# Kernel tuning notes

Measured on AMD Instinct MI355X. Metric: run time of the kernel, lower is better.

## Reference

```python
import jax, jax.numpy as jnp
import numpy as np

N = 8192      # nodes
DIN = 128     # in_channels
DH = 64       # hidden_channels (dim_out, num_heads=1)
DOUT = 32     # out_channels
RATIO = 0.5
K_KEEP = int(np.ceil(RATIO * N))  # SAGPooling keep count (single graph)
LN_EPS = 1e-5


def _linear_params(k, fan_in, fan_out):
    kw, kb = jax.random.split(k)
    W = jax.random.normal(kw, (fan_in, fan_out), dtype=jnp.float32) / jnp.sqrt(jnp.float32(fan_in))
    b = jax.random.normal(kb, (fan_out,), dtype=jnp.float32) * 0.01
    return W, b


def setup_inputs() -> dict:
    key = jax.random.key(0)
    ks = jax.random.split(key, 8)
    x = jax.random.normal(ks[0], (N, DIN), dtype=jnp.float32)
    batch = jnp.zeros((N,), dtype=jnp.int64)  # single graph
    Wq, bq = _linear_params(ks[1], DIN, DH)
    Wk, bk = _linear_params(ks[2], DIN, DH)
    Wv, bv = _linear_params(ks[3], DIN, DH)
    gcn_W, gcn_b = _linear_params(ks[4], DH, DH)       # GCNConv weight/bias
    score_W, score_b = _linear_params(ks[5], DH, 1)    # SAGPooling score GCNConv
    ln_g = jnp.ones((DH,), dtype=jnp.float32)
    ln_b = jnp.zeros((DH,), dtype=jnp.float32)
    head_W, head_b = _linear_params(ks[6], DH, DOUT)
    return dict(x=x, batch=batch, Wq=Wq, bq=bq, Wk=Wk, bk=bk, Wv=Wv, bv=bv,
                gcn_W=gcn_W, gcn_b=gcn_b, score_W=score_W, score_b=score_b,
                ln_g=ln_g, ln_b=ln_b, head_W=head_W, head_b=head_b)


def _forward(x, Wq, bq, Wk, bk, Wv, bv, gcn_W, gcn_b, score_W, score_b,
             ln_g, ln_b, head_W, head_b):
    # --- self-attention over all nodes (num_heads = 1) ---
    Q = x @ Wq + bq                                        # [N, DH]
    K = x @ Wk + bk
    V = x @ Wv + bv
    attn = jax.nn.softmax(Q @ K.T / jnp.sqrt(jnp.float32(DH)), axis=-1)  # [N, N]
    h = attn @ V                                           # [N, DH]

    # --- edge construction: threshold attention, ensure self-loops ---
    # (attn > 0.5).nonzero() -> edge set; empty -> self-loop fallback; then
    # add_self_loops. Dense equivalent: A = max(mask, I).
    eye = jnp.eye(N, dtype=x.dtype)
    A = jnp.maximum((attn > 0.5).astype(x.dtype), eye)     # [N, N], diag = 1

    # symmetric GCN normalization  D^{-1/2} A D^{-1/2}
    dinv = jax.lax.rsqrt(A.sum(axis=1))                    # [N]
    An = dinv[:, None] * A * dinv[None, :]                 # [N, N]

    # --- GCNConv layer ---
    g = An @ (h @ gcn_W) + gcn_b                           # [N, DH]

    # --- SAGPooling: GCNConv scorer -> tanh -> global top-k (single graph) ---
    score = jnp.tanh((An @ (g @ score_W) + score_b).squeeze(-1))  # [N]
    top_scores, perm = jax.lax.top_k(score, K_KEEP)        # sorted desc, like PyG topk
    xp = g[perm] * top_scores[:, None]                     # [K, DH], multiplier = 1

    # --- LayerNorm + ReLU (dropout is identity in eval) ---
    mu = xp.mean(axis=-1, keepdims=True)
    var = xp.var(axis=-1, keepdims=True)
    xp = (xp - mu) * jax.lax.rsqrt(var + LN_EPS) * ln_g + ln_b
    xp = jax.nn.relu(xp)

    # --- prediction head ---
    return xp @ head_W + head_b                            # [K, DOUT]


def reference(x, batch, Wq, bq, Wk, bk, Wv, bv, gcn_W, gcn_b,
              score_W, score_b, ln_g, ln_b, head_W, head_b):
    del batch  # single graph; grouping has no effect on the math
    return _forward(x, Wq, bq, Wk, bk, Wv, bv, gcn_W, gcn_b,
                    score_W, score_b, ln_g, ln_b, head_W, head_b)
```

## Files before the change

### kernel.cpp

```cpp
#include <hip/hip_runtime.h>
#include <hip/hip_bf16.h>
#include <cstdio>

typedef __hip_bfloat16 bf16;
typedef __attribute__((ext_vector_type(8))) short v8s;
typedef __attribute__((ext_vector_type(4))) short v4s;
typedef __attribute__((ext_vector_type(4))) float v4f;
typedef __attribute__((ext_vector_type(4))) double v4d;

#define MFMA16(a, b, c) __builtin_amdgcn_mfma_f32_16x16x32_bf16((a), (b), (c), 0, 0, 0)

#define NN 8192
#define DIN 128
#define DH 64
#define DOUT 32
#define KKEEP 4096
#define SPLITS 8
#define SPATT 8

__device__ __forceinline__ float bf2f(bf16 v) { return __bfloat162float(v); }
__device__ __forceinline__ short f2bfs(float f) {
  __hip_bfloat16 h = __float2bfloat16(f);
  return *reinterpret_cast<short*>(&h);
}
__device__ __forceinline__ bf16 f2bf(float v) { return __float2bfloat16(v); }

__device__ __forceinline__ double exp_d(double s) {
  const double L2E    = 1.4426950408889634074;
  const double LN2_HI = 6.93147180369123816490e-01;
  const double LN2_LO = 1.90821492927058770002e-10;
  double t  = s * L2E;
  double kf = rint(t);
  double r  = fma(-kf, LN2_HI, s);
  r = fma(-kf, LN2_LO, r);
  double p = 1.0 / 362880.0;
  p = fma(p, r, 1.0 / 40320.0);
  p = fma(p, r, 1.0 / 5040.0);
  p = fma(p, r, 1.0 / 720.0);
  p = fma(p, r, 1.0 / 120.0);
  p = fma(p, r, 1.0 / 24.0);
  p = fma(p, r, 1.0 / 6.0);
  p = fma(p, r, 0.5);
  p = fma(p, r, 1.0);
  p = fma(p, r, 1.0);
  int k = (int)kf;
  long long bits = ((long long)(1023 + k)) << 52;
  double sc = __longlong_as_double(bits);
  return p * sc;
}

__global__ void k0_ucb(const float* __restrict__ gW, const float* __restrict__ sW,
                       const float* __restrict__ gb, double* __restrict__ u) {
  int c = threadIdx.x;
  double acc = 0.0, accb = 0.0;
  for (int d = 0; d < DH; ++d) {
    double swd = (double)sW[d];
    acc  = fma((double)gW[c * DH + d], swd, acc);
    accb = fma((double)gb[d], swd, accb);
  }
  u[c] = acc;
  if (c == 0) u[64] = accb;
}

__global__ __launch_bounds__(256) void k1_prep(
    const float* __restrict__ x, const float* __restrict__ Wq, const float* __restrict__ bq,
    const float* __restrict__ Wk, const float* __restrict__ bk, const float* __restrict__ Wv,
    const float* __restrict__ bv, const double* __restrict__ u,
    double* __restrict__ Qd, double* __restrict__ Kd, double* __restrict__ w,
    bf16* __restrict__ Qb, bf16* __restrict__ Kb, bf16* __restrict__ Vt) {
  __shared__ double xs[16][DIN];
  int t = threadIdx.x;
  int nb = blockIdx.x * 16;
  for (int idx = t; idx < 16 * DIN; idx += 256)
    xs[idx >> 7][idx & 127] = (double)x[(size_t)nb * DIN + idx];
  __syncthreads();
  int d = t & 63;
  int sub = t >> 6;
  double bqd = (double)bq[d];
  double bkd = (double)bk[d];
  double bvd = (double)bv[d];
  double ud = u[d];
  for (int pass = 0; pass < 4; ++pass) {
    int n = pass * 4 + sub;
    double aq = bqd, ak = bkd, av = bvd;
#pragma unroll 8
    for (int c = 0; c < DIN; ++c) {
      double xv = xs[n][c];
      aq = fma(xv, (double)Wq[c * DH + d], aq);
      ak = fma(xv, (double)Wk[c * DH + d], ak);
      av = fma(xv, (double)Wv[c * DH + d], av);
    }
    aq *= 0.125;
    int node = nb + n;
    Qd[(size_t)node * DH + d] = aq;
    Kd[(size_t)node * DH + d] = ak;
    Qb[(size_t)node * DH + d] = f2bf((float)aq);
    Kb[(size_t)node * DH + d] = f2bf((float)ak);
    Vt[(size_t)d * NN + node] = f2bf((float)av);
    double pw = av * ud;
#pragma unroll
    for (int off = 32; off; off >>= 1) pw += __shfl_xor(pw, off);
    if (d == 0) w[node] = pw;
  }
}

__global__ __launch_bounds__(256) void k2_scores(
    const double* __restrict__ Qd, const double* __restrict__ Kd, const double* __restrict__ w,
    double* __restrict__ Zp, double* __restrict__ Wp, double* __restrict__ Ep, int* __restrict__ Jp) {
  __shared__ __align__(16) double Kbuf[2][32][66];
  const int t = threadIdx.x;
  const int wv = t >> 6;
  const int l = t & 63;
  const int li = l & 15, lg = l >> 4;
  const int rb = (blockIdx.x & 127) * 64;
  const int sp = blockIdx.x >> 7;
  const int cbeg = sp * (NN / SPLITS);

  double qreg[16];
  const double* qrow = Qd + (size_t)(rb + 16 * wv + li) * DH + lg;
#pragma unroll
  for (int tt = 0; tt < 16; ++tt) qreg[tt] = qrow[4 * tt];

  {
    const double* src = Kd + (size_t)cbeg * DH;
#pragma unroll
    for (int k = 0; k < 4; ++k) {
      int g = t + 256 * k;
      int r = g >> 5, c2 = g & 31;
      *(double2*)&Kbuf[0][r][c2 * 2] = *(const double2*)&src[r * DH + c2 * 2];
    }
  }
  __syncthreads();

  double Zt[4] = {0, 0, 0, 0}, Wt[4] = {0, 0, 0, 0}, Et[4] = {-1, -1, -1, -1};
  int Jt[4] = {0, 0, 0, 0};

  const int NT = (NN / SPLITS) / 32;
  for (int kt = 0; kt < NT; ++kt) {
    const int buf = kt & 1;
    if (kt + 1 < NT) {
      const double* src = Kd + (size_t)(cbeg + (kt + 1) * 32) * DH;
#pragma unroll
      for (int k = 0; k < 4; ++k) {
        int g = t + 256 * k;
        int r = g >> 5, c2 = g & 31;
        *(double2*)&Kbuf[buf ^ 1][r][c2 * 2] = *(const double2*)&src[r * DH + c2 * 2];
      }
    }
#pragma unroll
    for (int hf = 0; hf < 2; ++hf) {
      v4d acc = (v4d){0.0, 0.0, 0.0, 0.0};
#pragma unroll
      for (int tt = 0; tt < 16; ++tt) {
        double bfrag = Kbuf[buf][li + 16 * hf][4 * tt + lg];
        acc = __builtin_amdgcn_mfma_f64_16x16x4f64(qreg[tt], bfrag, acc, 0, 0, 0);
      }
      const int col = cbeg + kt * 32 + 16 * hf + li;
      const double wj = w[col];
#pragma unroll
      for (int v = 0; v < 4; ++v) {
        double e = exp_d(acc[v]);
        Zt[v] += e;
        Wt[v] = fma(e, wj, Wt[v]);
        if (e > Et[v]) { Et[v] = e; Jt[v] = col; }
      }
    }
    __syncthreads();
  }

#pragma unroll
  for (int v = 0; v < 4; ++v) {
#pragma unroll
    for (int m = 1; m < 16; m <<= 1) {
      Zt[v] += __shfl_xor(Zt[v], m);
      Wt[v] += __shfl_xor(Wt[v], m);
      double e2 = __shfl_xor(Et[v], m);
      int j2 = __shfl_xor(Jt[v], m);
      if (e2 > Et[v] || (e2 == Et[v] && j2 < Jt[v])) { Et[v] = e2; Jt[v] = j2; }
    }
  }
  if (li == 0) {
#pragma unroll
    for (int v = 0; v < 4; ++v) {
      int row = rb + 16 * wv + lg + 4 * v;
      Zp[sp * NN + row] = Zt[v];
      Wp[sp * NN + row] = Wt[v];
      Ep[sp * NN + row] = Et[v];
      Jp[sp * NN + row] = Jt[v];
    }
  }
}

__global__ void k3_combine(const double* __restrict__ Zp, const double* __restrict__ Wp,
                           const double* __restrict__ Ep, const int* __restrict__ Jp,
                           double* __restrict__ tau, int* __restrict__ extra, int* __restrict__ jmA) {
  int i = blockIdx.x * 256 + threadIdx.x;
  double Z = 0, W = 0, E = -1;
  int J = 0;
  for (int sp = 0; sp < SPLITS; ++sp) {
    Z += Zp[sp * NN + i];
    W += Wp[sp * NN + i];
    double e = Ep[sp * NN + i];
    if (e > E || (e == E && Jp[sp * NN + i] < J)) { E = e; J = Jp[sp * NN + i]; }
  }
  tau[i] = W / Z;
  extra[i] = (E > 0.5 * Z) && (J != i);
  jmA[i] = J & (NN - 1);
}

__global__ __launch_bounds__(256) void k4_mfma(const bf16* __restrict__ Qb, const bf16* __restrict__ Kb,
                                               const bf16* __restrict__ Vt,
                                               float* __restrict__ hp, float* __restrict__ zp) {
  __shared__ __align__(16) short P[4][16 * 40];
  const int t = threadIdx.x;
  const int wv = t >> 6;
  const int l = t & 63, g = l >> 4, li = l & 15;
  const int qb = (blockIdx.x & 127) * 64 + wv * 16;
  const int sp = blockIdx.x >> 7;
  short* Pw = &P[wv][0];
  const v8s q0 = *(const v8s*)(Qb + (size_t)(qb + li) * DH + g * 8);
  const v8s q1 = *(const v8s*)(Qb + (size_t)(qb + li) * DH + 32 + g * 8);
  v4f hacc[4];
#pragma unroll
  for (int db = 0; db < 4; ++db) hacc[db] = (v4f){0.f, 0.f, 0.f, 0.f};
  float zl = 0.f;
  const int kbeg = sp * (NN / SPATT);
  for (int jb = kbeg; jb < kbeg + NN / SPATT; jb += 32) {
    const bf16* kp = Kb + (size_t)(jb + li) * DH + g * 8;
    v8s ka0 = *(const v8s*)(kp);
    v8s ka1 = *(const v8s*)(kp + 32);
    v8s kb0 = *(const v8s*)(kp + 16 * DH);
    v8s kb1 = *(const v8s*)(kp + 16 * DH + 32);
    v4f c0 = (v4f){0.f, 0.f, 0.f, 0.f}, c1 = (v4f){0.f, 0.f, 0.f, 0.f};
    c0 = MFMA16(ka0, q0, c0);
    c0 = MFMA16(ka1, q1, c0);
    c1 = MFMA16(kb0, q0, c1);
    c1 = MFMA16(kb1, q1, c1);
    v4s p0, p1;
#pragma unroll
    for (int r = 0; r < 4; ++r) {
      short b0 = f2bfs(__expf(c0[r]));
      short b1 = f2bfs(__expf(c1[r]));
      p0[r] = b0;
      p1[r] = b1;
      zl += bf2f(*reinterpret_cast<bf16*>(&b0));
      zl += bf2f(*reinterpret_cast<bf16*>(&b1));
    }
    *(v4s*)&Pw[li * 40 + g * 4] = p0;
    *(v4s*)&Pw[li * 40 + 16 + g * 4] = p1;
    __syncthreads();
    v8s pf = *(const v8s*)&Pw[li * 40 + g * 8];
#pragma unroll
    for (int db = 0; db < 4; ++db) {
      const v8s vb = *(const v8s*)(Vt + (size_t)(db * 16 + li) * NN + jb + g * 8);
      hacc[db] = MFMA16(pf, vb, hacc[db]);
    }
    __syncthreads();
  }
  zl += __shfl_xor(zl, 16);
  zl += __shfl_xor(zl, 32);
  if (g == 0) zp[sp * NN + qb + li] = zl;
#pragma unroll
  for (int r = 0; r < 4; ++r) {
    int row = qb + g * 4 + r;
#pragma unroll
    for (int db = 0; db < 4; ++db)
      hp[((size_t)sp * NN + row) * DH + db * 16 + li] = hacc[db][r];
  }
}

__global__ __launch_bounds__(256) void k9_hM(const float* __restrict__ hp, const float* __restrict__ zp,
                                             const float* __restrict__ gW, float* __restrict__ M) {
  __shared__ float xs[4][DH];
  int t = threadIdx.x;
  int sub = t >> 6, d = t & 63;
  int n = blockIdx.x * 4 + sub;
  float Z = 0.f, H = 0.f;
#pragma unroll
  for (int sp = 0; sp < SPATT; ++sp) {
    Z += zp[sp * NN + n];
    H += hp[((size_t)sp * NN + n) * DH + d];
  }
  xs[sub][d] = H / Z;
  __syncthreads();
  float acc = 0.f;
#pragma unroll 8
  for (int c = 0; c < DH; ++c) acc = fmaf(xs[sub][c], gW[c * DH + d], acc);
  M[(size_t)n * DH + d] = acc;
}

__global__ void k5_t(const double* __restrict__ tau, const int* __restrict__ extra,
                     const int* __restrict__ jmA, const double* __restrict__ u, double* __restrict__ tarr) {
  int i = blockIdx.x * 256 + threadIdx.x;
  int ex = extra[i];
  double di = ex ? 0.70710678118654752440 : 1.0;
  double acc = di * tau[i];
  if (ex) {
    int j = jmA[i] & (NN - 1);
    double dj = extra[j] ? 0.70710678118654752440 : 1.0;
    acc = fma(dj, tau[j], acc);
  }
  tarr[i] = fma(di, acc, u[64]);
}

__global__ void k6_pre(const double* __restrict__ tarr, const int* __restrict__ extra,
                       const int* __restrict__ jmA, const float* __restrict__ score_b,
                       double* __restrict__ pre, float* __restrict__ sc32, int* __restrict__ cnt) {
  int i = blockIdx.x * 256 + threadIdx.x;
  int ex = extra[i];
  double di = ex ? 0.70710678118654752440 : 1.0;
  double acc = di * tarr[i];
  if (ex) {
    int j = jmA[i] & (NN - 1);
    double dj = extra[j] ? 0.70710678118654752440 : 1.0;
    acc = fma(dj, tarr[j], acc);
  }
  double p = fma(di, acc, (double)score_b[0]);
  pre[i] = p;
  sc32[i] = (float)tanh(p);
  cnt[i] = 0;
}

__global__ void k7_rank(const double* __restrict__ pre, int* __restrict__ cnt) {
  int i = (blockIdx.x & 31) * 256 + threadIdx.x;
  int j0 = (blockIdx.x >> 5) * 512;
  double si = pre[i];
  int c = 0;
#pragma unroll 4
  for (int j = j0; j < j0 + 512; j += 2) {
    double2 pj = *(const double2*)(pre + j);
    c += (pj.x > si || (pj.x == si && j < i));
    c += (pj.y > si || (pj.y == si && (j + 1) < i));
  }
  atomicAdd(&cnt[i], c);
}

__global__ void k8_sel(const int* __restrict__ cnt, int* __restrict__ sel) {
  int i = blockIdx.x * 256 + threadIdx.x;
  unsigned r = (unsigned)cnt[i];
  if (r < KKEEP) sel[r] = i;
}

__global__ __launch_bounds__(256) void k11_head(const float* __restrict__ M, const int* __restrict__ extra,
                                                const int* __restrict__ jmA, const float* __restrict__ gb,
                                                const float* __restrict__ sc32, const int* __restrict__ sel,
                                                const float* __restrict__ lg, const float* __restrict__ lb,
                                                const float* __restrict__ hW, const float* __restrict__ hb,
                                                float* __restrict__ out) {
  __shared__ float xs[4][DH];
  int t = threadIdx.x;
  int wv = t >> 6, d = t & 63;
  int p = blockIdx.x * 4 + wv;
  int i = sel[p] & (NN - 1);
  int ex = extra[i];
  float di = ex ? 0.70710678f : 1.0f;
  float acc0 = di * M[(size_t)i * DH + d];
  if (ex) {
    int j = jmA[i] & (NN - 1);
    acc0 = fmaf(extra[j] ? 0.70710678f : 1.0f, M[(size_t)j * DH + d], acc0);
  }
  float gval = fmaf(di, acc0, gb[d]);
  float v = gval * sc32[i];
  float s1 = v;
#pragma unroll
  for (int off = 32; off; off >>= 1) s1 += __shfl_xor(s1, off);
  float mu = s1 * (1.0f / 64.0f);
  float dv = v - mu;
  float s2 = dv * dv;
#pragma unroll
  for (int off = 32; off; off >>= 1) s2 += __shfl_xor(s2, off);
  float var = s2 * (1.0f / 64.0f);
  float xn = dv * rsqrtf(var + 1e-5f) * lg[d] + lb[d];
  xs[wv][d] = fmaxf(xn, 0.0f);
  __syncthreads();
  if (t < 128) {
    int r = t >> 5, o = t & 31;
    float acc = hb[o];
#pragma unroll 8
    for (int c = 0; c < DH; ++c) acc = fmaf(xs[r][c], hW[c * DOUT + o], acc);
    out[(size_t)(blockIdx.x * 4 + r) * DOUT + o] = acc;
  }
}

#define MB 1048576ull
constexpr size_t OFF_QD   = 0 * MB;
constexpr size_t OFF_KD   = 4 * MB;
constexpr size_t OFF_M    = 16 * MB;
constexpr size_t OFF_ZP   = 20 * MB;
constexpr size_t OFF_WP   = 21 * MB;
constexpr size_t OFF_EP   = 22 * MB;
constexpr size_t OFF_JP   = 23 * MB;
constexpr size_t OFF_W    = 24 * MB;
constexpr size_t OFF_U    = 25 * MB;
constexpr size_t OFF_TAU  = 26 * MB;
constexpr size_t OFF_EX   = 27 * MB;
constexpr size_t OFF_JM   = 28 * MB;
constexpr size_t OFF_T    = 29 * MB;
constexpr size_t OFF_PRE  = 30 * MB;
constexpr size_t OFF_SC   = 31 * MB;
constexpr size_t OFF_CNT  = 32 * MB;
constexpr size_t OFF_SEL  = 33 * MB;
constexpr size_t OFF_HP   = 34 * MB;
constexpr size_t OFF_ZATT = 50 * MB;
constexpr size_t OFF_QB   = 51 * MB;
constexpr size_t OFF_KB   = 52 * MB;
constexpr size_t OFF_VT   = 53 * MB;
constexpr size_t WS_NEEDED = 54 * MB;

extern "C" void kernel_launch(void* const* d_in, const int* in_sizes, int n_in,
                              void* d_out, int out_size, void* d_ws, size_t ws_size,
                              hipStream_t stream) {
  if (n_in < 16 || ws_size < WS_NEEDED || out_size != KKEEP * DOUT) {
    fprintf(stderr, "[sag] GUARD ws=%zu need=%zu n_in=%d out=%d\n", ws_size, WS_NEEDED, n_in, out_size);
    return;
  }
  const float* x   = (const float*)d_in[0];
  const float* Wq  = (const float*)d_in[2];
  const float* bq  = (const float*)d_in[3];
  const float* Wk  = (const float*)d_in[4];
  const float* bk  = (const float*)d_in[5];
  const float* Wv  = (const float*)d_in[6];
  const float* bv  = (const float*)d_in[7];
  const float* gW  = (const float*)d_in[8];
  const float* gb  = (const float*)d_in[9];
  const float* sW  = (const float*)d_in[10];
  const float* sb  = (const float*)d_in[11];
  const float* lg  = (const float*)d_in[12];
  const float* lb  = (const float*)d_in[13];
  const float* hW  = (const float*)d_in[14];
  const float* hb  = (const float*)d_in[15];
  float* out = (float*)d_out;

  char* ws = (char*)d_ws;
  double* Qd  = (double*)(ws + OFF_QD);
  double* Kd  = (double*)(ws + OFF_KD);
  bf16*   Qb  = (bf16*)(ws + OFF_QB);
  bf16*   Kb  = (bf16*)(ws + OFF_KB);
  bf16*   Vt  = (bf16*)(ws + OFF_VT);
  float*  M   = (float*)(ws + OFF_M);
  double* Zp  = (double*)(ws + OFF_ZP);
  double* Wp  = (double*)(ws + OFF_WP);
  double* Ep  = (double*)(ws + OFF_EP);
  int*    Jp  = (int*)(ws + OFF_JP);
  double* w   = (double*)(ws + OFF_W);
  double* u   = (double*)(ws + OFF_U);
  double* tau = (double*)(ws + OFF_TAU);
  int*    ex  = (int*)(ws + OFF_EX);
  int*    jm  = (int*)(ws + OFF_JM);
  double* tarr= (double*)(ws + OFF_T);
  double* pre = (double*)(ws + OFF_PRE);
  float*  sc32= (float*)(ws + OFF_SC);
  int*    cnt = (int*)(ws + OFF_CNT);
  int*    sel = (int*)(ws + OFF_SEL);
  float*  hp  = (float*)(ws + OFF_HP);
  float*  zatt= (float*)(ws + OFF_ZATT);

  hipLaunchKernelGGL(k0_ucb, dim3(1), dim3(64), 0, stream, gW, sW, gb, u);
  hipLaunchKernelGGL(k1_prep, dim3(512), dim3(256), 0, stream, x, Wq, bq, Wk, bk, Wv, bv, u,
                     Qd, Kd, w, Qb, Kb, Vt);
  hipLaunchKernelGGL(k2_scores, dim3(128 * SPLITS), dim3(256), 0, stream, Qd, Kd, w, Zp, Wp, Ep, Jp);
  hipLaunchKernelGGL(k3_combine, dim3(32), dim3(256), 0, stream, Zp, Wp, Ep, Jp, tau, ex, jm);
  hipLaunchKernelGGL(k4_mfma, dim3(128 * SPATT), dim3(256), 0, stream, Qb, Kb, Vt, hp, zatt);
  hipLaunchKernelGGL(k9_hM, dim3(2048), dim3(256), 0, stream, hp, zatt, gW, M);
  hipLaunchKernelGGL(k5_t, dim3(32), dim3(256), 0, stream, tau, ex, jm, u, tarr);
  hipLaunchKernelGGL(k6_pre, dim3(32), dim3(256), 0, stream, tarr, ex, jm, sb, pre, sc32, cnt);
  hipLaunchKernelGGL(k7_rank, dim3(512), dim3(256), 0, stream, pre, cnt);
  hipLaunchKernelGGL(k8_sel, dim3(32), dim3(256), 0, stream, cnt, sel);
  hipLaunchKernelGGL(k11_head, dim3(1024), dim3(256), 0, stream, M, ex, jm, gb, sc32, sel,
                     lg, lb, hW, hb, out);
}
```

Before: 407.5 us.

## Fuse fp64 score and bf16 attention kernels into one interleaved launch

Merges the fp64 MFMA score kernel and the bf16 attention-times-V kernel into one launch. Even blocks run the score work and odd blocks run the attention work, so the fp64-heavy and bf16-heavy blocks can share CUs at the same time. The fp64 path's K tile is halved from 32 to 16 rows so shared memory fits the common buffer, which doubles its loop trips and barriers. Occupancy may drop because register pressure is now the maximum of both paths.

After: 487.0 us. 1.19x slower.

```diff
diff --git a/kernel.cpp b/kernel.cpp
--- a/kernel.cpp
+++ b/kernel.cpp
@@ -104,58 +104,56 @@
   }
 }
 
-__global__ __launch_bounds__(256) void k2_scores(
+__global__ __launch_bounds__(256) void k24_fused(
     const double* __restrict__ Qd, const double* __restrict__ Kd, const double* __restrict__ w,
-    double* __restrict__ Zp, double* __restrict__ Wp, double* __restrict__ Ep, int* __restrict__ Jp) {
-  __shared__ __align__(16) double Kbuf[2][32][66];
+    double* __restrict__ Zp, double* __restrict__ Wp, double* __restrict__ Ep, int* __restrict__ Jp,
+    const bf16* __restrict__ Qb, const bf16* __restrict__ Kb, const bf16* __restrict__ Vt,
+    float* __restrict__ hp, float* __restrict__ zp) {
+  __shared__ __align__(16) char smem[16896];
   const int t = threadIdx.x;
   const int wv = t >> 6;
   const int l = t & 63;
-  const int li = l & 15, lg = l >> 4;
-  const int rb = (blockIdx.x & 127) * 64;
-  const int sp = blockIdx.x >> 7;
-  const int cbeg = sp * (NN / SPLITS);
-
-  double qreg[16];
-  const double* qrow = Qd + (size_t)(rb + 16 * wv + li) * DH + lg;
-#pragma unroll
-  for (int tt = 0; tt < 16; ++tt) qreg[tt] = qrow[4 * tt];
-
-  {
-    const double* src = Kd + (size_t)cbeg * DH;
-#pragma unroll
-    for (int k = 0; k < 4; ++k) {
-      int g = t + 256 * k;
-      int r = g >> 5, c2 = g & 31;
-      *(double2*)&Kbuf[0][r][c2 * 2] = *(const double2*)&src[r * DH + c2 * 2];
-    }
-  }
-  __syncthreads();
-
-  double Zt[4] = {0, 0, 0, 0}, Wt[4] = {0, 0, 0, 0}, Et[4] = {-1, -1, -1, -1};
-  int Jt[4] = {0, 0, 0, 0};
-
-  const int NT = (NN / SPLITS) / 32;
-  for (int kt = 0; kt < NT; ++kt) {
-    const int buf = kt & 1;
-    if (kt + 1 < NT) {
-      const double* src = Kd + (size_t)(cbeg + (kt + 1) * 32) * DH;
-#pragma unroll
-      for (int k = 0; k < 4; ++k) {
-        int g = t + 256 * k;
-        int r = g >> 5, c2 = g & 31;
-        *(double2*)&Kbuf[buf ^ 1][r][c2 * 2] = *(const double2*)&src[r * DH + c2 * 2];
-      }
-    }
-#pragma unroll
-    for (int hf = 0; hf < 2; ++hf) {
+  const int sub = blockIdx.x >> 1;
+
+  if ((blockIdx.x & 1) == 0) {
+    double (*Kbuf)[16][66] = (double (*)[16][66])smem;
+    const int li = l & 15, lg = l >> 4;
+    const int rb = (sub & 127) * 64;
+    const int sp = sub >> 7;
+    const int cbeg = sp * (NN / SPLITS);
+
+    double qreg[16];
+    const double* qrow = Qd + (size_t)(rb + 16 * wv + li) * DH + lg;
+#pragma unroll
+    for (int tt = 0; tt < 16; ++tt) qreg[tt] = qrow[4 * tt];
+
+    {
+      const double* src = Kd + (size_t)cbeg * DH;
+      int r = t >> 4, c = (t & 15) * 4;
+      *(double2*)&Kbuf[0][r][c]     = *(const double2*)&src[r * DH + c];
+      *(double2*)&Kbuf[0][r][c + 2] = *(const double2*)&src[r * DH + c + 2];
+    }
+    __syncthreads();
+
+    double Zt[4] = {0, 0, 0, 0}, Wt[4] = {0, 0, 0, 0}, Et[4] = {-1, -1, -1, -1};
+    int Jt[4] = {0, 0, 0, 0};
+
+    const int NT = (NN / SPLITS) / 16;
+    for (int kt = 0; kt < NT; ++kt) {
+      const int buf = kt & 1;
+      if (kt + 1 < NT) {
+        const double* src = Kd + (size_t)(cbeg + (kt + 1) * 16) * DH;
+        int r = t >> 4, c = (t & 15) * 4;
+        *(double2*)&Kbuf[buf ^ 1][r][c]     = *(const double2*)&src[r * DH + c];
+        *(double2*)&Kbuf[buf ^ 1][r][c + 2] = *(const double2*)&src[r * DH + c + 2];
+      }
       v4d acc = (v4d){0.0, 0.0, 0.0, 0.0};
 #pragma unroll
       for (int tt = 0; tt < 16; ++tt) {
-        double bfrag = Kbuf[buf][li + 16 * hf][4 * tt + lg];
+        double bfrag = Kbuf[buf][li][4 * tt + lg];
         acc = __builtin_amdgcn_mfma_f64_16x16x4f64(qreg[tt], bfrag, acc, 0, 0, 0);
       }
-      const int col = cbeg + kt * 32 + 16 * hf + li;
+      const int col = cbeg + kt * 16 + li;
       const double wj = w[col];
 #pragma unroll
       for (int v = 0; v < 4; ++v) {
@@ -164,29 +162,84 @@
         Wt[v] = fma(e, wj, Wt[v]);
         if (e > Et[v]) { Et[v] = e; Jt[v] = col; }
       }
-    }
-    __syncthreads();
-  }
-
-#pragma unroll
-  for (int v = 0; v < 4; ++v) {
-#pragma unroll
-    for (int m = 1; m < 16; m <<= 1) {
-      Zt[v] += __shfl_xor(Zt[v], m);
-      Wt[v] += __shfl_xor(Wt[v], m);
-      double e2 = __shfl_xor(Et[v], m);
-      int j2 = __shfl_xor(Jt[v], m);
-      if (e2 > Et[v] || (e2 == Et[v] && j2 < Jt[v])) { Et[v] = e2; Jt[v] = j2; }
-    }
-  }
-  if (li == 0) {
+      __syncthreads();
+    }
+
 #pragma unroll
     for (int v = 0; v < 4; ++v) {
-      int row = rb + 16 * wv + lg + 4 * v;
-      Zp[sp * NN + row] = Zt[v];
-      Wp[sp * NN + row] = Wt[v];
-      Ep[sp * NN + row] = Et[v];
-      Jp[sp * NN + row] = Jt[v];
+#pragma unroll
+      for (int m = 1; m < 16; m <<= 1) {
+        Zt[v] += __shfl_xor(Zt[v], m);
+        Wt[v] += __shfl_xor(Wt[v], m);
+        double e2 = __shfl_xor(Et[v], m);
+        int j2 = __shfl_xor(Jt[v], m);
+        if (e2 > Et[v] || (e2 == Et[v] && j2 < Jt[v])) { Et[v] = e2; Jt[v] = j2; }
+      }
+    }
+    if (li == 0) {
+#pragma unroll
+      for (int v = 0; v < 4; ++v) {
+        int row = rb + 16 * wv + lg + 4 * v;
+        Zp[sp * NN + row] = Zt[v];
+        Wp[sp * NN + row] = Wt[v];
+        Ep[sp * NN + row] = Et[v];
+        Jp[sp * NN + row] = Jt[v];
+      }
+    }
+  } else {
+    short (*P)[16 * 40] = (short (*)[16 * 40])smem;
+    const int g = l >> 4, li = l & 15;
+    const int qb = (sub & 127) * 64 + wv * 16;
+    const int sp = sub >> 7;
+    short* Pw = &P[wv][0];
+    const v8s q0 = *(const v8s*)(Qb + (size_t)(qb + li) * DH + g * 8);
+    const v8s q1 = *(const v8s*)(Qb + (size_t)(qb + li) * DH + 32 + g * 8);
+    v4f hacc[4];
+#pragma unroll
+    for (int db = 0; db < 4; ++db) hacc[db] = (v4f){0.f, 0.f, 0.f, 0.f};
+    float zl = 0.f;
+    const int kbeg = sp * (NN / SPATT);
+    for (int jb = kbeg; jb < kbeg + NN / SPATT; jb += 32) {
+      const bf16* kp = Kb + (size_t)(jb + li) * DH + g * 8;
+      v8s ka0 = *(const v8s*)(kp);
+      v8s ka1 = *(const v8s*)(kp + 32);
+      v8s kb0 = *(const v8s*)(kp + 16 * DH);
+      v8s kb1 = *(const v8s*)(kp + 16 * DH + 32);
+      v4f c0 = (v4f){0.f, 0.f, 0.f, 0.f}, c1 = (v4f){0.f, 0.f, 0.f, 0.f};
+      c0 = MFMA16(ka0, q0, c0);
+      c0 = MFMA16(ka1, q1, c0);
+      c1 = MFMA16(kb0, q0, c1);
+      c1 = MFMA16(kb1, q1, c1);
+      v4s p0, p1;
+#pragma unroll
+      for (int r = 0; r < 4; ++r) {
+        short b0 = f2bfs(__expf(c0[r]));
+        short b1 = f2bfs(__expf(c1[r]));
+        p0[r] = b0;
+        p1[r] = b1;
+        zl += bf2f(*reinterpret_cast<bf16*>(&b0));
+        zl += bf2f(*reinterpret_cast<bf16*>(&b1));
+      }
+      *(v4s*)&Pw[li * 40 + g * 4] = p0;
+      *(v4s*)&Pw[li * 40 + 16 + g * 4] = p1;
+      __syncthreads();
+      v8s pf = *(const v8s*)&Pw[li * 40 + g * 8];
+#pragma unroll
+      for (int db = 0; db < 4; ++db) {
+        const v8s vb = *(const v8s*)(Vt + (size_t)(db * 16 + li) * NN + jb + g * 8);
+        hacc[db] = MFMA16(pf, vb, hacc[db]);
+      }
+      __syncthreads();
+    }
+    zl += __shfl_xor(zl, 16);
+    zl += __shfl_xor(zl, 32);
+    if (g == 0) zp[sp * NN + qb + li] = zl;
+#pragma unroll
+    for (int r = 0; r < 4; ++r) {
+      int row = qb + g * 4 + r;
+#pragma unroll
+      for (int db = 0; db < 4; ++db)
+        hp[((size_t)sp * NN + row) * DH + db * 16 + li] = hacc[db][r];
     }
   }
 }
@@ -206,67 +259,6 @@
   tau[i] = W / Z;
   extra[i] = (E > 0.5 * Z) && (J != i);
   jmA[i] = J & (NN - 1);
-}
-
-__global__ __launch_bounds__(256) void k4_mfma(const bf16* __restrict__ Qb, const bf16* __restrict__ Kb,
-                                               const bf16* __restrict__ Vt,
-                                               float* __restrict__ hp, float* __restrict__ zp) {
-  __shared__ __align__(16) short P[4][16 * 40];
-  const int t = threadIdx.x;
-  const int wv = t >> 6;
-  const int l = t & 63, g = l >> 4, li = l & 15;
-  const int qb = (blockIdx.x & 127) * 64 + wv * 16;
-  const int sp = blockIdx.x >> 7;
-  short* Pw = &P[wv][0];
-  const v8s q0 = *(const v8s*)(Qb + (size_t)(qb + li) * DH + g * 8);
-  const v8s q1 = *(const v8s*)(Qb + (size_t)(qb + li) * DH + 32 + g * 8);
-  v4f hacc[4];
-#pragma unroll
-  for (int db = 0; db < 4; ++db) hacc[db] = (v4f){0.f, 0.f, 0.f, 0.f};
-  float zl = 0.f;
-  const int kbeg = sp * (NN / SPATT);
-  for (int jb = kbeg; jb < kbeg + NN / SPATT; jb += 32) {
-    const bf16* kp = Kb + (size_t)(jb + li) * DH + g * 8;
-    v8s ka0 = *(const v8s*)(kp);
-    v8s ka1 = *(const v8s*)(kp + 32);
-    v8s kb0 = *(const v8s*)(kp + 16 * DH);
-    v8s kb1 = *(const v8s*)(kp + 16 * DH + 32);
-    v4f c0 = (v4f){0.f, 0.f, 0.f, 0.f}, c1 = (v4f){0.f, 0.f, 0.f, 0.f};
-    c0 = MFMA16(ka0, q0, c0);
-    c0 = MFMA16(ka1, q1, c0);
-    c1 = MFMA16(kb0, q0, c1);
-    c1 = MFMA16(kb1, q1, c1);
-    v4s p0, p1;
-#pragma unroll
-    for (int r = 0; r < 4; ++r) {
-      short b0 = f2bfs(__expf(c0[r]));
-      short b1 = f2bfs(__expf(c1[r]));
-      p0[r] = b0;
-      p1[r] = b1;
-      zl += bf2f(*reinterpret_cast<bf16*>(&b0));
-      zl += bf2f(*reinterpret_cast<bf16*>(&b1));
-    }
-    *(v4s*)&Pw[li * 40 + g * 4] = p0;
-    *(v4s*)&Pw[li * 40 + 16 + g * 4] = p1;
-    __syncthreads();
-    v8s pf = *(const v8s*)&Pw[li * 40 + g * 8];
-#pragma unroll
-    for (int db = 0; db < 4; ++db) {
-      const v8s vb = *(const v8s*)(Vt + (size_t)(db * 16 + li) * NN + jb + g * 8);
-      hacc[db] = MFMA16(pf, vb, hacc[db]);
-    }
-    __syncthreads();
-  }
-  zl += __shfl_xor(zl, 16);
-  zl += __shfl_xor(zl, 32);
-  if (g == 0) zp[sp * NN + qb + li] = zl;
-#pragma unroll
-  for (int r = 0; r < 4; ++r) {
-    int row = qb + g * 4 + r;
-#pragma unroll
-    for (int db = 0; db < 4; ++db)
-      hp[((size_t)sp * NN + row) * DH + db * 16 + li] = hacc[db][r];
-  }
 }
 
 __global__ __launch_bounds__(256) void k9_hM(const float* __restrict__ hp, const float* __restrict__ zp,
@@ -458,10 +450,10 @@
   hipLaunchKernelGGL(k0_ucb, dim3(1), dim3(64), 0, stream, gW, sW, gb, u);
   hipLaunchKernelGGL(k1_prep, dim3(512), dim3(256), 0, stream, x, Wq, bq, Wk, bk, Wv, bv, u,
                      Qd, Kd, w, Qb, Kb, Vt);
-  hipLaunchKernelGGL(k2_scores, dim3(128 * SPLITS), dim3(256), 0, stream, Qd, Kd, w, Zp, Wp, Ep, Jp);
+  hipLaunchKernelGGL(k24_fused, dim3(2048), dim3(256), 0, stream,
+                     Qd, Kd, w, Zp, Wp, Ep, Jp, Qb, Kb, Vt, hp, zatt);
+  hipLaunchKernelGGL(k9_hM, dim3(2048), dim3(256), 0, stream, hp, zatt, gW, M);
   hipLaunchKernelGGL(k3_combine, dim3(32), dim3(256), 0, stream, Zp, Wp, Ep, Jp, tau, ex, jm);
-  hipLaunchKernelGGL(k4_mfma, dim3(128 * SPATT), dim3(256), 0, stream, Qb, Kb, Vt, hp, zatt);
-  hipLaunchKernelGGL(k9_hM, dim3(2048), dim3(256), 0, stream, hp, zatt, gW, M);
   hipLaunchKernelGGL(k5_t, dim3(32), dim3(256), 0, stream, tau, ex, jm, u, tarr);
   hipLaunchKernelGGL(k6_pre, dim3(32), dim3(256), 0, stream, tarr, ex, jm, sb, pre, sc32, cnt);
   hipLaunchKernelGGL(k7_rank, dim3(512), dim3(256), 0, stream, pre, cnt);
```
